# Kernel tuning notes

Measured on AMD Instinct MI355X. Metric: run time of the kernel, lower is better.

The kernel has to match this reference:

```python
import jax, jax.numpy as jnp
import numpy as np

N_NODES = 100000
N_EDGES = 3_200_000
F_IN, HID, N_CLS = 512, 16, 16


def setup_inputs() -> dict:
    key = jax.random.key(0)
    k1, k2, k3, k4 = jax.random.split(key, 4)
    x = jax.random.normal(k1, (N_NODES, F_IN), dtype=jnp.float32)
    edge_index = jax.random.randint(k2, (2, N_EDGES), 0, N_NODES, dtype=jnp.int64)
    W1 = jax.random.normal(k3, (F_IN, HID), dtype=jnp.float32) * 0.05
    b1 = jnp.zeros((HID,), dtype=jnp.float32)
    W2 = jax.random.normal(k4, (HID, N_CLS), dtype=jnp.float32) * 0.05
    b2 = jnp.zeros((N_CLS,), dtype=jnp.float32)
    return {"x": x, "edge_index": edge_index, "W1": W1, "b1": b1, "W2": W2, "b2": b2}


def _gcn_conv(x, W, b, row, col, norm, n_nodes):
    # GCNConv: linear first, then symmetric-normalized scatter-add aggregation
    h = x @ W                              # [N, out]
    msg = h[row] * norm[:, None]           # gather + scale, [E+N, out]
    out = jax.ops.segment_sum(msg, col, num_segments=n_nodes)
    return out + b


def reference(x, edge_index, W1, b1, W2, b2):
    n = x.shape[0]
    # add self-loops (GCNConv default)
    loop = jnp.arange(n, dtype=edge_index.dtype)
    row = jnp.concatenate([edge_index[0], loop])
    col = jnp.concatenate([edge_index[1], loop])
    # symmetric normalization D^-1/2 A D^-1/2 with edge_weight = 1
    deg = jax.ops.segment_sum(jnp.ones_like(col, dtype=x.dtype), col, num_segments=n)
    dinv = jnp.where(deg > 0, deg ** -0.5, 0.0)
    norm = dinv[row] * dinv[col]

    h = jax.nn.relu(_gcn_conv(x, W1, b1, row, col, norm, n))
    # dropout is identity in eval mode
    out = _gcn_conv(h, W2, b2, row, col, norm, n)
    return jax.nn.log_softmax(out, axis=-1)
```

## Files before the change

### kernel.cpp

```cpp
#include <hip/hip_runtime.h>
#include <hip/hip_fp16.h>

#define F_IN 512
#define BKT_BITS 7
#define NPB (1 << BKT_BITS)
#define NBMAX 1024
#define BWIN 5120
#define EPT 32
#define EPW (256 * EPT)

__global__ void k_init(int* __restrict__ cursor, int nb) {
    int i = blockIdx.x * blockDim.x + threadIdx.x;
    if (i < nb) cursor[i] = i * BWIN;
}

__global__ __launch_bounds__(256) void k_part(
    const int* __restrict__ row, const int* __restrict__ col,
    int* __restrict__ cursor, unsigned int* __restrict__ pairs, int E, int nb)
{
    __shared__ unsigned int staged[EPW];
    __shared__ unsigned short bkt[EPW];
    __shared__ int hist[NBMAX];
    __shared__ int sc[NBMAX];
    __shared__ int base[NBMAX];
    __shared__ int wsum[4];
    int tid = threadIdx.x;
    int lane = tid & 63;
    int e0 = blockIdx.x * EPW;
    for (int i = tid; i < nb; i += 256) hist[i] = 0;
    __syncthreads();

    int4 c4[EPT / 4];
    int rank[EPT];
    #pragma unroll
    for (int k = 0; k < EPT / 4; ++k) {
        int e = e0 + (tid + k * 256) * 4;
        if (e + 3 < E) {
            c4[k] = ((const int4*)col)[e >> 2];
        } else {
            c4[k].x = (e     < E) ? col[e]     : -1;
            c4[k].y = (e + 1 < E) ? col[e + 1] : -1;
            c4[k].z = (e + 2 < E) ? col[e + 2] : -1;
            c4[k].w = (e + 3 < E) ? col[e + 3] : -1;
        }
        const int* cc = (const int*)&c4[k];
        #pragma unroll
        for (int i = 0; i < 4; ++i)
            rank[4 * k + i] = (cc[i] >= 0) ? atomicAdd(&hist[cc[i] >> BKT_BITS], 1) : 0;
    }
    __syncthreads();

    int i0 = tid * 4;
    int a0 = 0, a1 = 0, a2 = 0, a3 = 0;
    {
        int h0 = (i0     < nb) ? hist[i0]     : 0;
        int h1 = (i0 + 1 < nb) ? hist[i0 + 1] : 0;
        int h2 = (i0 + 2 < nb) ? hist[i0 + 2] : 0;
        int h3 = (i0 + 3 < nb) ? hist[i0 + 3] : 0;
        base[i0]     = h0 ? atomicAdd(&cursor[i0],     h0) : 0;
        if (i0 + 1 < NBMAX) base[i0 + 1] = h1 ? atomicAdd(&cursor[i0 + 1], h1) : 0;
        if (i0 + 2 < NBMAX) base[i0 + 2] = h2 ? atomicAdd(&cursor[i0 + 2], h2) : 0;
        if (i0 + 3 < NBMAX) base[i0 + 3] = h3 ? atomicAdd(&cursor[i0 + 3], h3) : 0;
        a0 = h0; a1 = h1; a2 = h2; a3 = h3;
    }
    int s = a0 + a1 + a2 + a3;
    int ws = s;
    #pragma unroll
    for (int off = 1; off < 64; off <<= 1) {
        int t = __shfl_up(ws, off);
        if (lane >= off) ws += t;
    }
    if (lane == 63) wsum[tid >> 6] = ws;
    __syncthreads();
    int woff = 0;
    #pragma unroll
    for (int k = 0; k < 4; ++k) woff += (k < (tid >> 6)) ? wsum[k] : 0;
    int excl = woff + ws - s;
    sc[i0]     = excl + a0;
    sc[i0 + 1] = excl + a0 + a1;
    sc[i0 + 2] = excl + a0 + a1 + a2;
    sc[i0 + 3] = excl + s;
    __syncthreads();

    #pragma unroll
    for (int k = 0; k < EPT / 4; ++k) {
        int e = e0 + (tid + k * 256) * 4;
        int4 r4;
        if (e + 3 < E) {
            r4 = ((const int4*)row)[e >> 2];
        } else {
            r4.x = (e     < E) ? row[e]     : 0;
            r4.y = (e + 1 < E) ? row[e + 1] : 0;
            r4.z = (e + 2 < E) ? row[e + 2] : 0;
            r4.w = (e + 3 < E) ? row[e + 3] : 0;
        }
        const int* cc = (const int*)&c4[k];
        const int* rr = (const int*)&r4;
        #pragma unroll
        for (int i = 0; i < 4; ++i) {
            if (e + i >= E || cc[i] < 0) continue;
            int b = cc[i] >> BKT_BITS;
            int pos = (sc[b] - hist[b]) + rank[4 * k + i];
            staged[pos] = ((unsigned int)rr[i] << BKT_BITS)
                        | (unsigned int)(cc[i] & (NPB - 1));
            bkt[pos] = (unsigned short)b;
        }
    }
    __syncthreads();

    int vcnt = sc[nb - 1];
    for (int i = tid; i < vcnt; i += 256) {
        int b = bkt[i];
        int gpos = base[b] + (i - (sc[b] - hist[b]));
        if (gpos < (b + 1) * BWIN)
            pairs[gpos] = staged[i];
    }
}

__global__ __launch_bounds__(256) void k_csr(
    unsigned int* __restrict__ pairs, const int* __restrict__ cursor,
    int2* __restrict__ pd, float* __restrict__ dinv, int n, int nb)
{
    __shared__ int sorted[BWIN];
    __shared__ int hist[NPB];
    __shared__ int sc[NPB];
    __shared__ int curs[NPB];
    int b = blockIdx.x, tid = threadIdx.x;
    int n0 = b << BKT_BITS;
    int w0 = b * BWIN;
    int ec = min(cursor[b] - w0, BWIN);
    if (tid < NPB) hist[tid] = 0;
    __syncthreads();
    for (int e4 = tid; e4 < BWIN / 4; e4 += 256) {
        uint4 p4 = ((const uint4*)(pairs + w0))[e4];
        int e = e4 * 4;
        const unsigned int* pp = (const unsigned int*)&p4;
        #pragma unroll
        for (int i = 0; i < 4; ++i)
            if (e + i < ec) atomicAdd(&hist[pp[i] & (NPB - 1)], 1);
    }
    __syncthreads();
    if (tid < NPB) sc[tid] = hist[tid];
    __syncthreads();
    for (int off = 1; off < NPB; off <<= 1) {
        int t = (tid < NPB && tid >= off) ? sc[tid - off] : 0;
        __syncthreads();
        if (tid < NPB) sc[tid] += t;
        __syncthreads();
    }
    if (tid < NPB) {
        int st = sc[tid] - hist[tid];
        curs[tid] = st;
        int node = n0 + tid;
        if (node < n) {
            pd[node] = make_int2(w0 + st, hist[tid]);
            dinv[node] = rsqrtf((float)(hist[tid] + 1));
        }
    }
    __syncthreads();
    for (int e4 = tid; e4 < BWIN / 4; e4 += 256) {
        uint4 p4 = ((const uint4*)(pairs + w0))[e4];
        int e = e4 * 4;
        const unsigned int* pp = (const unsigned int*)&p4;
        #pragma unroll
        for (int i = 0; i < 4; ++i) {
            if (e + i < ec) {
                unsigned int p = pp[i];
                int pos = atomicAdd(&curs[p & (NPB - 1)], 1);
                sorted[pos] = (int)(p >> BKT_BITS);
            }
        }
    }
    __syncthreads();
    for (int i = tid; i < ec; i += 256)
        ((int*)pairs)[w0 + i] = sorted[i];
}

__global__ __launch_bounds__(256) void k_gemm1(
    const float* __restrict__ x, const float* __restrict__ W1,
    const float* __restrict__ dinv, __half2* __restrict__ hs, int n)
{
    __shared__ float red[4][64 * 17];
    const int lane = threadIdx.x & 63;
    const int wib  = threadIdx.x >> 6;
    const int wave = blockIdx.x * 4 + wib;
    const int nw   = gridDim.x * 4;
    float* rb = red[wib];

    float w[128];
    #pragma unroll
    for (int i = 0; i < 32; ++i) {
        float4 t = ((const float4*)W1)[lane * 32 + i];
        w[4*i+0] = t.x; w[4*i+1] = t.y; w[4*i+2] = t.z; w[4*i+3] = t.w;
    }
    const int q  = lane >> 4;
    const int jj = lane & 15;

    int node = wave;
    float4 a = {}, b = {};
    float di = 0.f;
    if (node < n) {
        const float4* xr = (const float4*)(x + (size_t)node * F_IN);
        a = xr[lane * 2];
        b = xr[lane * 2 + 1];
        di = dinv[node];
    }
    while (node < n) {
        int nxt = node + nw;
        float4 an = {}, bn = {};
        float dn = 0.f;
        if (nxt < n) {
            const float4* xr = (const float4*)(x + (size_t)nxt * F_IN);
            an = xr[lane * 2];
            bn = xr[lane * 2 + 1];
            dn = dinv[nxt];
        }
        float xs[8] = {a.x, a.y, a.z, a.w, b.x, b.y, b.z, b.w};
        float p[16];
        #pragma unroll
        for (int j = 0; j < 16; ++j) p[j] = 0.f;
        #pragma unroll
        for (int i = 0; i < 8; ++i)
            #pragma unroll
            for (int j = 0; j < 16; ++j)
                p[j] = fmaf(xs[i], w[i * 16 + j], p[j]);

        #pragma unroll
        for (int j = 0; j < 16; ++j) rb[lane * 17 + j] = p[j];
        __asm__ volatile("s_waitcnt lgkmcnt(0)" ::: "memory");
        float s = 0.f;
        #pragma unroll
        for (int i = 0; i < 16; ++i) s += rb[(q * 16 + i) * 17 + jj];
        s += __shfl_down(s, 32);
        s += __shfl_down(s, 16);

        float sv = s * di;
        float sn = __shfl_down(sv, 1);
        if (lane < 16 && (lane & 1) == 0) {
            __half2 hv = __halves2half2(__float2half(sv), __float2half(sn));
            hs[node * 8 + (lane >> 1)] = hv;
        }
        node = nxt; a = an; b = bn; di = dn;
    }
}

__global__ __launch_bounds__(256) void k_agg1(
    const __half2* __restrict__ hs, const int2* __restrict__ pd,
    const int* __restrict__ csr, const float* __restrict__ dinv,
    const float* __restrict__ b1, const float* __restrict__ W2,
    __half2* __restrict__ hs2, int n)
{
    int t = blockIdx.x * blockDim.x + threadIdx.x;
    int node = t >> 3, j2 = t & 7;
    if (node >= n) return;
    int2 p = pd[node];
    int e = p.x, s1 = p.x + p.y;
    float2 sum = __half22float2(hs[node * 8 + j2]);
    for (; e + 8 <= s1; e += 8) {
        int a0 = csr[e],   a1 = csr[e+1], a2 = csr[e+2], a3 = csr[e+3];
        int a4 = csr[e+4], a5 = csr[e+5], a6 = csr[e+6], a7 = csr[e+7];
        float2 v0 = __half22float2(hs[a0 * 8 + j2]);
        float2 v1 = __half22float2(hs[a1 * 8 + j2]);
        float2 v2 = __half22float2(hs[a2 * 8 + j2]);
        float2 v3 = __half22float2(hs[a3 * 8 + j2]);
        float2 v4 = __half22float2(hs[a4 * 8 + j2]);
        float2 v5 = __half22float2(hs[a5 * 8 + j2]);
        float2 v6 = __half22float2(hs[a6 * 8 + j2]);
        float2 v7 = __half22float2(hs[a7 * 8 + j2]);
        sum.x += ((v0.x+v1.x)+(v2.x+v3.x)) + ((v4.x+v5.x)+(v6.x+v7.x));
        sum.y += ((v0.y+v1.y)+(v2.y+v3.y)) + ((v4.y+v5.y)+(v6.y+v7.y));
    }
    for (; e < s1; ++e) {
        float2 v = __half22float2(hs[csr[e] * 8 + j2]);
        sum.x += v.x; sum.y += v.y;
    }
    float di = dinv[node];
    float2 b1v = ((const float2*)b1)[j2];
    float va = fmaxf(fmaf(sum.x, di, b1v.x), 0.f);
    float vb = fmaxf(fmaf(sum.y, di, b1v.y), 0.f);
    float ha = 0.f, hb = 0.f;
    #pragma unroll
    for (int k2 = 0; k2 < 8; ++k2) {
        float oa = __shfl(va, k2, 8);
        float ob = __shfl(vb, k2, 8);
        ha = fmaf(oa, W2[(2*k2)   * 16 + 2*j2],     ha);
        hb = fmaf(oa, W2[(2*k2)   * 16 + 2*j2 + 1], hb);
        ha = fmaf(ob, W2[(2*k2+1) * 16 + 2*j2],     ha);
        hb = fmaf(ob, W2[(2*k2+1) * 16 + 2*j2 + 1], hb);
    }
    hs2[node * 8 + j2] = __halves2half2(__float2half(ha * di), __float2half(hb * di));
}

__global__ __launch_bounds__(256) void k_agg2(
    const __half2* __restrict__ hs2, const int2* __restrict__ pd,
    const int* __restrict__ csr, const float* __restrict__ dinv,
    const float* __restrict__ b2, float2* __restrict__ out, int n)
{
    int t = blockIdx.x * blockDim.x + threadIdx.x;
    int node = t >> 3, j2 = t & 7;
    if (node >= n) return;
    int2 p = pd[node];
    int e = p.x, s1 = p.x + p.y;
    float2 sum = __half22float2(hs2[node * 8 + j2]);
    for (; e + 8 <= s1; e += 8) {
        int a0 = csr[e],   a1 = csr[e+1], a2 = csr[e+2], a3 = csr[e+3];
        int a4 = csr[e+4], a5 = csr[e+5], a6 = csr[e+6], a7 = csr[e+7];
        float2 v0 = __half22float2(hs2[a0 * 8 + j2]);
        float2 v1 = __half22float2(hs2[a1 * 8 + j2]);
        float2 v2 = __half22float2(hs2[a2 * 8 + j2]);
        float2 v3 = __half22float2(hs2[a3 * 8 + j2]);
        float2 v4 = __half22float2(hs2[a4 * 8 + j2]);
        float2 v5 = __half22float2(hs2[a5 * 8 + j2]);
        float2 v6 = __half22float2(hs2[a6 * 8 + j2]);
        float2 v7 = __half22float2(hs2[a7 * 8 + j2]);
        sum.x += ((v0.x+v1.x)+(v2.x+v3.x)) + ((v4.x+v5.x)+(v6.x+v7.x));
        sum.y += ((v0.y+v1.y)+(v2.y+v3.y)) + ((v4.y+v5.y)+(v6.y+v7.y));
    }
    for (; e < s1; ++e) {
        float2 v = __half22float2(hs2[csr[e] * 8 + j2]);
        sum.x += v.x; sum.y += v.y;
    }
    float di = dinv[node];
    float2 b2v = ((const float2*)b2)[j2];
    float vx = fmaf(sum.x, di, b2v.x);
    float vy = fmaf(sum.y, di, b2v.y);
    float m = fmaxf(vx, vy);
    #pragma unroll
    for (int off = 4; off >= 1; off >>= 1) m = fmaxf(m, __shfl_xor(m, off));
    float s = expf(vx - m) + expf(vy - m);
    #pragma unroll
    for (int off = 4; off >= 1; off >>= 1) s += __shfl_xor(s, off);
    float ls = logf(s);
    out[node * 8 + j2] = make_float2(vx - m - ls, vy - m - ls);
}

extern "C" void kernel_launch(void* const* d_in, const int* in_sizes, int n_in,
                              void* d_out, int out_size, void* d_ws, size_t ws_size,
                              hipStream_t stream)
{
    const float* x  = (const float*)d_in[0];
    const int*   ei = (const int*)d_in[1];
    const float* W1 = (const float*)d_in[2];
    const float* b1 = (const float*)d_in[3];
    const float* W2 = (const float*)d_in[4];
    const float* b2 = (const float*)d_in[5];
    float* out = (float*)d_out;

    const int n = in_sizes[0] / F_IN;
    const int E = in_sizes[1] / 2;
    const int nb = (n + NPB - 1) >> BKT_BITS;

    char* ws = (char*)d_ws;
    size_t o = 0;
    #define ALIGN512(s) (((s) + 511) & ~(size_t)511)
    float* dinv = (float*)(ws + o);           o += ALIGN512((size_t)n * 4);
    int2*  pd   = (int2*)(ws + o);            o += ALIGN512((size_t)n * 8);
    int*   curs = (int*)(ws + o);             o += ALIGN512((size_t)NBMAX * 4);
    unsigned int* pairs = (unsigned int*)(ws + o);
    o += ALIGN512((size_t)nb * BWIN * 4);
    __half2* hs  = (__half2*)(ws + o);        o += ALIGN512((size_t)n * 16 * 2);
    __half2* hs2 = (__half2*)(ws + o);        o += ALIGN512((size_t)n * 16 * 2);
    #undef ALIGN512

    k_init<<<(nb + 255) / 256, 256, 0, stream>>>(curs, nb);
    k_part<<<(E + EPW - 1) / EPW, 256, 0, stream>>>(ei, ei + E, curs, pairs, E, nb);
    k_csr <<<nb, 256, 0, stream>>>(pairs, curs, pd, dinv, n, nb);

    k_gemm1<<<2048, 256, 0, stream>>>(x, W1, dinv, hs, n);
    k_agg1 <<<(n * 8 + 255) / 256, 256, 0, stream>>>(hs, pd, (const int*)pairs,
                                                     dinv, b1, W2, hs2, n);
    k_agg2 <<<(n * 8 + 255) / 256, 256, 0, stream>>>(hs2, pd, (const int*)pairs,
                                                     dinv, b2, (float2*)out, n);
}
```

Baseline: 434.7 us.

## Fuse all stages into one persistent kernel with software grid barriers

Replaces the six separate launches (init, partition, CSR build, GEMM, two aggregations) with one persistent kernel. It sizes the grid from occupancy and separates phases with an atomic-counter grid barrier, and shared memory is unioned across phases. Cursor init becomes a memset, with cursors now relative to each bucket. The aim is to remove launch gaps and tail effects between stages. In exchange, the partition and GEMM phases run on fewer blocks, register pressure rises under launch_bounds(256,2), and the software barrier adds its own cost and a deadlock risk if not all blocks are co-resident.

```diff
diff --git a/kernel.cpp b/kernel.cpp
--- a/kernel.cpp
+++ b/kernel.cpp
@@ -9,329 +9,352 @@
 #define EPT 32
 #define EPW (256 * EPT)
 
-__global__ void k_init(int* __restrict__ cursor, int nb) {
-    int i = blockIdx.x * blockDim.x + threadIdx.x;
-    if (i < nb) cursor[i] = i * BWIN;
+union SU {
+    struct {
+        unsigned int staged[EPW];
+        unsigned short bkt[EPW];
+        int hist[NBMAX];
+        int sc[NBMAX];
+        int base[NBMAX];
+        int wsum[4];
+    } p;
+    struct {
+        int sorted[BWIN];
+        int hist[NPB];
+        int sc[NPB];
+        int curs[NPB];
+    } c;
+    struct {
+        float red[4][64 * 17];
+    } g;
+};
+
+__device__ __forceinline__ void gbar(int* cnt, int* gen, int nblk) {
+    __syncthreads();
+    if (threadIdx.x == 0) {
+        __threadfence();
+        int g = __hip_atomic_load(gen, __ATOMIC_RELAXED, __HIP_MEMORY_SCOPE_AGENT);
+        if (__hip_atomic_fetch_add(cnt, 1, __ATOMIC_RELAXED,
+                                   __HIP_MEMORY_SCOPE_AGENT) == nblk - 1) {
+            __hip_atomic_store(cnt, 0, __ATOMIC_RELAXED, __HIP_MEMORY_SCOPE_AGENT);
+            __hip_atomic_store(gen, g + 1, __ATOMIC_RELEASE, __HIP_MEMORY_SCOPE_AGENT);
+        } else {
+            while (__hip_atomic_load(gen, __ATOMIC_RELAXED,
+                                     __HIP_MEMORY_SCOPE_AGENT) == g)
+                __builtin_amdgcn_s_sleep(8);
+        }
+        __threadfence();
+    }
+    __syncthreads();
 }
 
-__global__ __launch_bounds__(256) void k_part(
-    const int* __restrict__ row, const int* __restrict__ col,
-    int* __restrict__ cursor, unsigned int* __restrict__ pairs, int E, int nb)
+__global__ __launch_bounds__(256, 2) void k_fused(
+    const float* __restrict__ x, const int* __restrict__ ei,
+    const float* __restrict__ W1, const float* __restrict__ b1,
+    const float* __restrict__ W2, const float* __restrict__ b2,
+    float2* __restrict__ out,
+    float* __restrict__ dinv, int2* __restrict__ pd, int* __restrict__ cursor,
+    int* __restrict__ bar, unsigned int* __restrict__ pairs,
+    __half2* __restrict__ hs, __half2* __restrict__ hs2,
+    int n, int E, int nb, int nslice)
 {
-    __shared__ unsigned int staged[EPW];
-    __shared__ unsigned short bkt[EPW];
-    __shared__ int hist[NBMAX];
-    __shared__ int sc[NBMAX];
-    __shared__ int base[NBMAX];
-    __shared__ int wsum[4];
-    int tid = threadIdx.x;
-    int lane = tid & 63;
-    int e0 = blockIdx.x * EPW;
-    for (int i = tid; i < nb; i += 256) hist[i] = 0;
-    __syncthreads();
-
-    int4 c4[EPT / 4];
-    int rank[EPT];
-    #pragma unroll
-    for (int k = 0; k < EPT / 4; ++k) {
-        int e = e0 + (tid + k * 256) * 4;
-        if (e + 3 < E) {
-            c4[k] = ((const int4*)col)[e >> 2];
-        } else {
-            c4[k].x = (e     < E) ? col[e]     : -1;
-            c4[k].y = (e + 1 < E) ? col[e + 1] : -1;
-            c4[k].z = (e + 2 < E) ? col[e + 2] : -1;
-            c4[k].w = (e + 3 < E) ? col[e + 3] : -1;
-        }
-        const int* cc = (const int*)&c4[k];
+    __shared__ SU sh;
+    const int tid  = threadIdx.x;
+    const int lane = tid & 63;
+    const int gsz  = gridDim.x * 256;
+    const int* row = ei;
+    const int* col = ei + E;
+
+    for (int s = blockIdx.x; s < nslice; s += gridDim.x) {
+        int e0 = s * EPW;
+        for (int i = tid; i < nb; i += 256) sh.p.hist[i] = 0;
+        __syncthreads();
+
+        int4 c4[EPT / 4];
+        int rank[EPT];
         #pragma unroll
-        for (int i = 0; i < 4; ++i)
-            rank[4 * k + i] = (cc[i] >= 0) ? atomicAdd(&hist[cc[i] >> BKT_BITS], 1) : 0;
-    }
-    __syncthreads();
-
-    int i0 = tid * 4;
-    int a0 = 0, a1 = 0, a2 = 0, a3 = 0;
+        for (int k = 0; k < EPT / 4; ++k) {
+            int e = e0 + (tid + k * 256) * 4;
+            if (e + 3 < E) {
+                c4[k] = ((const int4*)col)[e >> 2];
+            } else {
+                c4[k].x = (e     < E) ? col[e]     : -1;
+                c4[k].y = (e + 1 < E) ? col[e + 1] : -1;
+                c4[k].z = (e + 2 < E) ? col[e + 2] : -1;
+                c4[k].w = (e + 3 < E) ? col[e + 3] : -1;
+            }
+            const int* cc = (const int*)&c4[k];
+            #pragma unroll
+            for (int i = 0; i < 4; ++i)
+                rank[4 * k + i] = (cc[i] >= 0)
+                    ? atomicAdd(&sh.p.hist[cc[i] >> BKT_BITS], 1) : 0;
+        }
+        __syncthreads();
+
+        int i0 = tid * 4;
+        int h0 = (i0     < nb) ? sh.p.hist[i0]     : 0;
+        int h1 = (i0 + 1 < nb) ? sh.p.hist[i0 + 1] : 0;
+        int h2 = (i0 + 2 < nb) ? sh.p.hist[i0 + 2] : 0;
+        int h3 = (i0 + 3 < nb) ? sh.p.hist[i0 + 3] : 0;
+        sh.p.base[i0]     = h0 ? i0 * BWIN       + atomicAdd(&cursor[i0],     h0) : 0;
+        sh.p.base[i0 + 1] = h1 ? (i0 + 1) * BWIN + atomicAdd(&cursor[i0 + 1], h1) : 0;
+        sh.p.base[i0 + 2] = h2 ? (i0 + 2) * BWIN + atomicAdd(&cursor[i0 + 2], h2) : 0;
+        sh.p.base[i0 + 3] = h3 ? (i0 + 3) * BWIN + atomicAdd(&cursor[i0 + 3], h3) : 0;
+        int ssum = h0 + h1 + h2 + h3;
+        int ws = ssum;
+        #pragma unroll
+        for (int off = 1; off < 64; off <<= 1) {
+            int t = __shfl_up(ws, off);
+            if (lane >= off) ws += t;
+        }
+        if (lane == 63) sh.p.wsum[tid >> 6] = ws;
+        __syncthreads();
+        int woff = 0;
+        #pragma unroll
+        for (int k = 0; k < 4; ++k) woff += (k < (tid >> 6)) ? sh.p.wsum[k] : 0;
+        int excl = woff + ws - ssum;
+        sh.p.sc[i0]     = excl + h0;
+        sh.p.sc[i0 + 1] = excl + h0 + h1;
+        sh.p.sc[i0 + 2] = excl + h0 + h1 + h2;
+        sh.p.sc[i0 + 3] = excl + ssum;
+        __syncthreads();
+
+        #pragma unroll
+        for (int k = 0; k < EPT / 4; ++k) {
+            int e = e0 + (tid + k * 256) * 4;
+            int4 r4;
+            if (e + 3 < E) {
+                r4 = ((const int4*)row)[e >> 2];
+            } else {
+                r4.x = (e     < E) ? row[e]     : 0;
+                r4.y = (e + 1 < E) ? row[e + 1] : 0;
+                r4.z = (e + 2 < E) ? row[e + 2] : 0;
+                r4.w = (e + 3 < E) ? row[e + 3] : 0;
+            }
+            const int* cc = (const int*)&c4[k];
+            const int* rr = (const int*)&r4;
+            #pragma unroll
+            for (int i = 0; i < 4; ++i) {
+                if (e + i >= E || cc[i] < 0) continue;
+                int b = cc[i] >> BKT_BITS;
+                int pos = (sh.p.sc[b] - sh.p.hist[b]) + rank[4 * k + i];
+                sh.p.staged[pos] = ((unsigned int)rr[i] << BKT_BITS)
+                                 | (unsigned int)(cc[i] & (NPB - 1));
+                sh.p.bkt[pos] = (unsigned short)b;
+            }
+        }
+        __syncthreads();
+
+        int vcnt = sh.p.sc[nb - 1];
+        for (int i = tid; i < vcnt; i += 256) {
+            int b = sh.p.bkt[i];
+            int gpos = sh.p.base[b] + (i - (sh.p.sc[b] - sh.p.hist[b]));
+            if (gpos < (b + 1) * BWIN)
+                pairs[gpos] = sh.p.staged[i];
+        }
+        __syncthreads();
+    }
+    gbar(bar, bar + 1, gridDim.x);
+
+    for (int b = blockIdx.x; b < nb; b += gridDim.x) {
+        int n0 = b << BKT_BITS;
+        int w0 = b * BWIN;
+        int ec = min(cursor[b], BWIN);
+        if (tid < NPB) sh.c.hist[tid] = 0;
+        __syncthreads();
+        for (int e4 = tid; e4 < BWIN / 4; e4 += 256) {
+            uint4 p4 = ((const uint4*)(pairs + w0))[e4];
+            int e = e4 * 4;
+            const unsigned int* pp = (const unsigned int*)&p4;
+            #pragma unroll
+            for (int i = 0; i < 4; ++i)
+                if (e + i < ec) atomicAdd(&sh.c.hist[pp[i] & (NPB - 1)], 1);
+        }
+        __syncthreads();
+        if (tid < NPB) sh.c.sc[tid] = sh.c.hist[tid];
+        __syncthreads();
+        for (int off = 1; off < NPB; off <<= 1) {
+            int t = (tid < NPB && tid >= off) ? sh.c.sc[tid - off] : 0;
+            __syncthreads();
+            if (tid < NPB) sh.c.sc[tid] += t;
+            __syncthreads();
+        }
+        if (tid < NPB) {
+            int st = sh.c.sc[tid] - sh.c.hist[tid];
+            sh.c.curs[tid] = st;
+            int node = n0 + tid;
+            if (node < n) {
+                pd[node] = make_int2(w0 + st, sh.c.hist[tid]);
+                dinv[node] = rsqrtf((float)(sh.c.hist[tid] + 1));
+            }
+        }
+        __syncthreads();
+        for (int e4 = tid; e4 < BWIN / 4; e4 += 256) {
+            uint4 p4 = ((const uint4*)(pairs + w0))[e4];
+            int e = e4 * 4;
+            const unsigned int* pp = (const unsigned int*)&p4;
+            #pragma unroll
+            for (int i = 0; i < 4; ++i) {
+                if (e + i < ec) {
+                    unsigned int p = pp[i];
+                    int pos = atomicAdd(&sh.c.curs[p & (NPB - 1)], 1);
+                    sh.c.sorted[pos] = (int)(p >> BKT_BITS);
+                }
+            }
+        }
+        __syncthreads();
+        for (int i = tid; i < ec; i += 256)
+            ((int*)pairs)[w0 + i] = sh.c.sorted[i];
+        __syncthreads();
+    }
+    gbar(bar, bar + 1, gridDim.x);
+
     {
-        int h0 = (i0     < nb) ? hist[i0]     : 0;
-        int h1 = (i0 + 1 < nb) ? hist[i0 + 1] : 0;
-        int h2 = (i0 + 2 < nb) ? hist[i0 + 2] : 0;
-        int h3 = (i0 + 3 < nb) ? hist[i0 + 3] : 0;
-        base[i0]     = h0 ? atomicAdd(&cursor[i0],     h0) : 0;
-        if (i0 + 1 < NBMAX) base[i0 + 1] = h1 ? atomicAdd(&cursor[i0 + 1], h1) : 0;
-        if (i0 + 2 < NBMAX) base[i0 + 2] = h2 ? atomicAdd(&cursor[i0 + 2], h2) : 0;
-        if (i0 + 3 < NBMAX) base[i0 + 3] = h3 ? atomicAdd(&cursor[i0 + 3], h3) : 0;
-        a0 = h0; a1 = h1; a2 = h2; a3 = h3;
-    }
-    int s = a0 + a1 + a2 + a3;
-    int ws = s;
-    #pragma unroll
-    for (int off = 1; off < 64; off <<= 1) {
-        int t = __shfl_up(ws, off);
-        if (lane >= off) ws += t;
-    }
-    if (lane == 63) wsum[tid >> 6] = ws;
-    __syncthreads();
-    int woff = 0;
-    #pragma unroll
-    for (int k = 0; k < 4; ++k) woff += (k < (tid >> 6)) ? wsum[k] : 0;
-    int excl = woff + ws - s;
-    sc[i0]     = excl + a0;
-    sc[i0 + 1] = excl + a0 + a1;
-    sc[i0 + 2] = excl + a0 + a1 + a2;
-    sc[i0 + 3] = excl + s;
-    __syncthreads();
-
-    #pragma unroll
-    for (int k = 0; k < EPT / 4; ++k) {
-        int e = e0 + (tid + k * 256) * 4;
-        int4 r4;
-        if (e + 3 < E) {
-            r4 = ((const int4*)row)[e >> 2];
-        } else {
-            r4.x = (e     < E) ? row[e]     : 0;
-            r4.y = (e + 1 < E) ? row[e + 1] : 0;
-            r4.z = (e + 2 < E) ? row[e + 2] : 0;
-            r4.w = (e + 3 < E) ? row[e + 3] : 0;
-        }
-        const int* cc = (const int*)&c4[k];
-        const int* rr = (const int*)&r4;
+        const int wib = tid >> 6;
+        float* rb = sh.g.red[wib];
+        float w[128];
         #pragma unroll
-        for (int i = 0; i < 4; ++i) {
-            if (e + i >= E || cc[i] < 0) continue;
-            int b = cc[i] >> BKT_BITS;
-            int pos = (sc[b] - hist[b]) + rank[4 * k + i];
-            staged[pos] = ((unsigned int)rr[i] << BKT_BITS)
-                        | (unsigned int)(cc[i] & (NPB - 1));
-            bkt[pos] = (unsigned short)b;
-        }
-    }
-    __syncthreads();
-
-    int vcnt = sc[nb - 1];
-    for (int i = tid; i < vcnt; i += 256) {
-        int b = bkt[i];
-        int gpos = base[b] + (i - (sc[b] - hist[b]));
-        if (gpos < (b + 1) * BWIN)
-            pairs[gpos] = staged[i];
-    }
-}
-
-__global__ __launch_bounds__(256) void k_csr(
-    unsigned int* __restrict__ pairs, const int* __restrict__ cursor,
-    int2* __restrict__ pd, float* __restrict__ dinv, int n, int nb)
-{
-    __shared__ int sorted[BWIN];
-    __shared__ int hist[NPB];
-    __shared__ int sc[NPB];
-    __shared__ int curs[NPB];
-    int b = blockIdx.x, tid = threadIdx.x;
-    int n0 = b << BKT_BITS;
-    int w0 = b * BWIN;
-    int ec = min(cursor[b] - w0, BWIN);
-    if (tid < NPB) hist[tid] = 0;
-    __syncthreads();
-    for (int e4 = tid; e4 < BWIN / 4; e4 += 256) {
-        uint4 p4 = ((const uint4*)(pairs + w0))[e4];
-        int e = e4 * 4;
-        const unsigned int* pp = (const unsigned int*)&p4;
-        #pragma unroll
-        for (int i = 0; i < 4; ++i)
-            if (e + i < ec) atomicAdd(&hist[pp[i] & (NPB - 1)], 1);
-    }
-    __syncthreads();
-    if (tid < NPB) sc[tid] = hist[tid];
-    __syncthreads();
-    for (int off = 1; off < NPB; off <<= 1) {
-        int t = (tid < NPB && tid >= off) ? sc[tid - off] : 0;
-        __syncthreads();
-        if (tid < NPB) sc[tid] += t;
-        __syncthreads();
-    }
-    if (tid < NPB) {
-        int st = sc[tid] - hist[tid];
-        curs[tid] = st;
-        int node = n0 + tid;
+        for (int i = 0; i < 32; ++i) {
+            float4 t = ((const float4*)W1)[lane * 32 + i];
+            w[4*i+0] = t.x; w[4*i+1] = t.y; w[4*i+2] = t.z; w[4*i+3] = t.w;
+        }
+        const int q  = lane >> 4;
+        const int jj = lane & 15;
+        const int nw = gridDim.x * 4;
+
+        int node = blockIdx.x * 4 + wib;
+        float4 a = {}, b = {};
+        float di = 0.f;
         if (node < n) {
-            pd[node] = make_int2(w0 + st, hist[tid]);
-            dinv[node] = rsqrtf((float)(hist[tid] + 1));
-        }
-    }
-    __syncthreads();
-    for (int e4 = tid; e4 < BWIN / 4; e4 += 256) {
-        uint4 p4 = ((const uint4*)(pairs + w0))[e4];
-        int e = e4 * 4;
-        const unsigned int* pp = (const unsigned int*)&p4;
-        #pragma unroll
-        for (int i = 0; i < 4; ++i) {
-            if (e + i < ec) {
-                unsigned int p = pp[i];
-                int pos = atomicAdd(&curs[p & (NPB - 1)], 1);
-                sorted[pos] = (int)(p >> BKT_BITS);
-            }
-        }
-    }
-    __syncthreads();
-    for (int i = tid; i < ec; i += 256)
-        ((int*)pairs)[w0 + i] = sorted[i];
-}
-
-__global__ __launch_bounds__(256) void k_gemm1(
-    const float* __restrict__ x, const float* __restrict__ W1,
-    const float* __restrict__ dinv, __half2* __restrict__ hs, int n)
-{
-    __shared__ float red[4][64 * 17];
-    const int lane = threadIdx.x & 63;
-    const int wib  = threadIdx.x >> 6;
-    const int wave = blockIdx.x * 4 + wib;
-    const int nw   = gridDim.x * 4;
-    float* rb = red[wib];
-
-    float w[128];
-    #pragma unroll
-    for (int i = 0; i < 32; ++i) {
-        float4 t = ((const float4*)W1)[lane * 32 + i];
-        w[4*i+0] = t.x; w[4*i+1] = t.y; w[4*i+2] = t.z; w[4*i+3] = t.w;
-    }
-    const int q  = lane >> 4;
-    const int jj = lane & 15;
-
-    int node = wave;
-    float4 a = {}, b = {};
-    float di = 0.f;
-    if (node < n) {
-        const float4* xr = (const float4*)(x + (size_t)node * F_IN);
-        a = xr[lane * 2];
-        b = xr[lane * 2 + 1];
-        di = dinv[node];
-    }
-    while (node < n) {
-        int nxt = node + nw;
-        float4 an = {}, bn = {};
-        float dn = 0.f;
-        if (nxt < n) {
-            const float4* xr = (const float4*)(x + (size_t)nxt * F_IN);
-            an = xr[lane * 2];
-            bn = xr[lane * 2 + 1];
-            dn = dinv[nxt];
-        }
-        float xs[8] = {a.x, a.y, a.z, a.w, b.x, b.y, b.z, b.w};
-        float p[16];
-        #pragma unroll
-        for (int j = 0; j < 16; ++j) p[j] = 0.f;
-        #pragma unroll
-        for (int i = 0; i < 8; ++i)
-            #pragma unroll
-            for (int j = 0; j < 16; ++j)
-                p[j] = fmaf(xs[i], w[i * 16 + j], p[j]);
-
-        #pragma unroll
-        for (int j = 0; j < 16; ++j) rb[lane * 17 + j] = p[j];
-        __asm__ volatile("s_waitcnt lgkmcnt(0)" ::: "memory");
-        float s = 0.f;
-        #pragma unroll
-        for (int i = 0; i < 16; ++i) s += rb[(q * 16 + i) * 17 + jj];
-        s += __shfl_down(s, 32);
-        s += __shfl_down(s, 16);
-
-        float sv = s * di;
-        float sn = __shfl_down(sv, 1);
-        if (lane < 16 && (lane & 1) == 0) {
-            __half2 hv = __halves2half2(__float2half(sv), __float2half(sn));
-            hs[node * 8 + (lane >> 1)] = hv;
-        }
-        node = nxt; a = an; b = bn; di = dn;
-    }
-}
-
-__global__ __launch_bounds__(256) void k_agg1(
-    const __half2* __restrict__ hs, const int2* __restrict__ pd,
-    const int* __restrict__ csr, const float* __restrict__ dinv,
-    const float* __restrict__ b1, const float* __restrict__ W2,
-    __half2* __restrict__ hs2, int n)
-{
-    int t = blockIdx.x * blockDim.x + threadIdx.x;
-    int node = t >> 3, j2 = t & 7;
-    if (node >= n) return;
-    int2 p = pd[node];
-    int e = p.x, s1 = p.x + p.y;
-    float2 sum = __half22float2(hs[node * 8 + j2]);
-    for (; e + 8 <= s1; e += 8) {
-        int a0 = csr[e],   a1 = csr[e+1], a2 = csr[e+2], a3 = csr[e+3];
-        int a4 = csr[e+4], a5 = csr[e+5], a6 = csr[e+6], a7 = csr[e+7];
-        float2 v0 = __half22float2(hs[a0 * 8 + j2]);
-        float2 v1 = __half22float2(hs[a1 * 8 + j2]);
-        float2 v2 = __half22float2(hs[a2 * 8 + j2]);
-        float2 v3 = __half22float2(hs[a3 * 8 + j2]);
-        float2 v4 = __half22float2(hs[a4 * 8 + j2]);
-        float2 v5 = __half22float2(hs[a5 * 8 + j2]);
-        float2 v6 = __half22float2(hs[a6 * 8 + j2]);
-        float2 v7 = __half22float2(hs[a7 * 8 + j2]);
-        sum.x += ((v0.x+v1.x)+(v2.x+v3.x)) + ((v4.x+v5.x)+(v6.x+v7.x));
-        sum.y += ((v0.y+v1.y)+(v2.y+v3.y)) + ((v4.y+v5.y)+(v6.y+v7.y));
-    }
-    for (; e < s1; ++e) {
-        float2 v = __half22float2(hs[csr[e] * 8 + j2]);
-        sum.x += v.x; sum.y += v.y;
-    }
-    float di = dinv[node];
-    float2 b1v = ((const float2*)b1)[j2];
-    float va = fmaxf(fmaf(sum.x, di, b1v.x), 0.f);
-    float vb = fmaxf(fmaf(sum.y, di, b1v.y), 0.f);
-    float ha = 0.f, hb = 0.f;
-    #pragma unroll
-    for (int k2 = 0; k2 < 8; ++k2) {
-        float oa = __shfl(va, k2, 8);
-        float ob = __shfl(vb, k2, 8);
-        ha = fmaf(oa, W2[(2*k2)   * 16 + 2*j2],     ha);
-        hb = fmaf(oa, W2[(2*k2)   * 16 + 2*j2 + 1], hb);
-        ha = fmaf(ob, W2[(2*k2+1) * 16 + 2*j2],     ha);
-        hb = fmaf(ob, W2[(2*k2+1) * 16 + 2*j2 + 1], hb);
-    }
-    hs2[node * 8 + j2] = __halves2half2(__float2half(ha * di), __float2half(hb * di));
-}
-
-__global__ __launch_bounds__(256) void k_agg2(
-    const __half2* __restrict__ hs2, const int2* __restrict__ pd,
-    const int* __restrict__ csr, const float* __restrict__ dinv,
-    const float* __restrict__ b2, float2* __restrict__ out, int n)
-{
-    int t = blockIdx.x * blockDim.x + threadIdx.x;
-    int node = t >> 3, j2 = t & 7;
-    if (node >= n) return;
-    int2 p = pd[node];
-    int e = p.x, s1 = p.x + p.y;
-    float2 sum = __half22float2(hs2[node * 8 + j2]);
-    for (; e + 8 <= s1; e += 8) {
-        int a0 = csr[e],   a1 = csr[e+1], a2 = csr[e+2], a3 = csr[e+3];
-        int a4 = csr[e+4], a5 = csr[e+5], a6 = csr[e+6], a7 = csr[e+7];
-        float2 v0 = __half22float2(hs2[a0 * 8 + j2]);
-        float2 v1 = __half22float2(hs2[a1 * 8 + j2]);
-        float2 v2 = __half22float2(hs2[a2 * 8 + j2]);
-        float2 v3 = __half22float2(hs2[a3 * 8 + j2]);
-        float2 v4 = __half22float2(hs2[a4 * 8 + j2]);
-        float2 v5 = __half22float2(hs2[a5 * 8 + j2]);
-        float2 v6 = __half22float2(hs2[a6 * 8 + j2]);
-        float2 v7 = __half22float2(hs2[a7 * 8 + j2]);
-        sum.x += ((v0.x+v1.x)+(v2.x+v3.x)) + ((v4.x+v5.x)+(v6.x+v7.x));
-        sum.y += ((v0.y+v1.y)+(v2.y+v3.y)) + ((v4.y+v5.y)+(v6.y+v7.y));
-    }
-    for (; e < s1; ++e) {
-        float2 v = __half22float2(hs2[csr[e] * 8 + j2]);
-        sum.x += v.x; sum.y += v.y;
-    }
-    float di = dinv[node];
-    float2 b2v = ((const float2*)b2)[j2];
-    float vx = fmaf(sum.x, di, b2v.x);
-    float vy = fmaf(sum.y, di, b2v.y);
-    float m = fmaxf(vx, vy);
-    #pragma unroll
-    for (int off = 4; off >= 1; off >>= 1) m = fmaxf(m, __shfl_xor(m, off));
-    float s = expf(vx - m) + expf(vy - m);
-    #pragma unroll
-    for (int off = 4; off >= 1; off >>= 1) s += __shfl_xor(s, off);
-    float ls = logf(s);
-    out[node * 8 + j2] = make_float2(vx - m - ls, vy - m - ls);
+            const float4* xr = (const float4*)(x + (size_t)node * F_IN);
+            a = xr[lane * 2];
+            b = xr[lane * 2 + 1];
+            di = dinv[node];
+        }
+        while (node < n) {
+            int nxt = node + nw;
+            float4 an = {}, bn = {};
+            float dn = 0.f;
+            if (nxt < n) {
+                const float4* xr = (const float4*)(x + (size_t)nxt * F_IN);
+                an = xr[lane * 2];
+                bn = xr[lane * 2 + 1];
+                dn = dinv[nxt];
+            }
+            float xs[8] = {a.x, a.y, a.z, a.w, b.x, b.y, b.z, b.w};
+            float p[16];
+            #pragma unroll
+            for (int j = 0; j < 16; ++j) p[j] = 0.f;
+            #pragma unroll
+            for (int i = 0; i < 8; ++i)
+                #pragma unroll
+                for (int j = 0; j < 16; ++j)
+                    p[j] = fmaf(xs[i], w[i * 16 + j], p[j]);
+
+            #pragma unroll
+            for (int j = 0; j < 16; ++j) rb[lane * 17 + j] = p[j];
+            __asm__ volatile("s_waitcnt lgkmcnt(0)" ::: "memory");
+            float s = 0.f;
+            #pragma unroll
+            for (int i = 0; i < 16; ++i) s += rb[(q * 16 + i) * 17 + jj];
+            s += __shfl_down(s, 32);
+            s += __shfl_down(s, 16);
+
+            float sv = s * di;
+            float sn = __shfl_down(sv, 1);
+            if (lane < 16 && (lane & 1) == 0) {
+                __half2 hv = __halves2half2(__float2half(sv), __float2half(sn));
+                hs[node * 8 + (lane >> 1)] = hv;
+            }
+            node = nxt; a = an; b = bn; di = dn;
+        }
+    }
+    gbar(bar, bar + 1, gridDim.x);
+
+    {
+        const int* csr = (const int*)pairs;
+        for (int it = blockIdx.x * 256 + tid; it < n * 8; it += gsz) {
+            int node = it >> 3, j2 = it & 7;
+            int2 p = pd[node];
+            int e = p.x, s1 = p.x + p.y;
+            float2 sum = __half22float2(hs[node * 8 + j2]);
+            for (; e + 8 <= s1; e += 8) {
+                int a0 = csr[e],   a1 = csr[e+1], a2 = csr[e+2], a3 = csr[e+3];
+                int a4 = csr[e+4], a5 = csr[e+5], a6 = csr[e+6], a7 = csr[e+7];
+                float2 v0 = __half22float2(hs[a0 * 8 + j2]);
+                float2 v1 = __half22float2(hs[a1 * 8 + j2]);
+                float2 v2 = __half22float2(hs[a2 * 8 + j2]);
+                float2 v3 = __half22float2(hs[a3 * 8 + j2]);
+                float2 v4 = __half22float2(hs[a4 * 8 + j2]);
+                float2 v5 = __half22float2(hs[a5 * 8 + j2]);
+                float2 v6 = __half22float2(hs[a6 * 8 + j2]);
+                float2 v7 = __half22float2(hs[a7 * 8 + j2]);
+                sum.x += ((v0.x+v1.x)+(v2.x+v3.x)) + ((v4.x+v5.x)+(v6.x+v7.x));
+                sum.y += ((v0.y+v1.y)+(v2.y+v3.y)) + ((v4.y+v5.y)+(v6.y+v7.y));
+            }
+            for (; e < s1; ++e) {
+                float2 v = __half22float2(hs[csr[e] * 8 + j2]);
+                sum.x += v.x; sum.y += v.y;
+            }
+            float di = dinv[node];
+            float2 b1v = ((const float2*)b1)[j2];
+            float va = fmaxf(fmaf(sum.x, di, b1v.x), 0.f);
+            float vb = fmaxf(fmaf(sum.y, di, b1v.y), 0.f);
+            float ha = 0.f, hb = 0.f;
+            #pragma unroll
+            for (int k2 = 0; k2 < 8; ++k2) {
+                float oa = __shfl(va, k2, 8);
+                float ob = __shfl(vb, k2, 8);
+                ha = fmaf(oa, W2[(2*k2)   * 16 + 2*j2],     ha);
+                hb = fmaf(oa, W2[(2*k2)   * 16 + 2*j2 + 1], hb);
+                ha = fmaf(ob, W2[(2*k2+1) * 16 + 2*j2],     ha);
+                hb = fmaf(ob, W2[(2*k2+1) * 16 + 2*j2 + 1], hb);
+            }
+            hs2[node * 8 + j2] =
+                __halves2half2(__float2half(ha * di), __float2half(hb * di));
+        }
+    }
+    gbar(bar, bar + 1, gridDim.x);
+
+    {
+        const int* csr = (const int*)pairs;
+        for (int it = blockIdx.x * 256 + tid; it < n * 8; it += gsz) {
+            int node = it >> 3, j2 = it & 7;
+            int2 p = pd[node];
+            int e = p.x, s1 = p.x + p.y;
+            float2 sum = __half22float2(hs2[node * 8 + j2]);
+            for (; e + 8 <= s1; e += 8) {
+                int a0 = csr[e],   a1 = csr[e+1], a2 = csr[e+2], a3 = csr[e+3];
+                int a4 = csr[e+4], a5 = csr[e+5], a6 = csr[e+6], a7 = csr[e+7];
+                float2 v0 = __half22float2(hs2[a0 * 8 + j2]);
+                float2 v1 = __half22float2(hs2[a1 * 8 + j2]);
+                float2 v2 = __half22float2(hs2[a2 * 8 + j2]);
+                float2 v3 = __half22float2(hs2[a3 * 8 + j2]);
+                float2 v4 = __half22float2(hs2[a4 * 8 + j2]);
+                float2 v5 = __half22float2(hs2[a5 * 8 + j2]);
+                float2 v6 = __half22float2(hs2[a6 * 8 + j2]);
+                float2 v7 = __half22float2(hs2[a7 * 8 + j2]);
+                sum.x += ((v0.x+v1.x)+(v2.x+v3.x)) + ((v4.x+v5.x)+(v6.x+v7.x));
+                sum.y += ((v0.y+v1.y)+(v2.y+v3.y)) + ((v4.y+v5.y)+(v6.y+v7.y));
+            }
+            for (; e < s1; ++e) {
+                float2 v = __half22float2(hs2[csr[e] * 8 + j2]);
+                sum.x += v.x; sum.y += v.y;
+            }
+            float di = dinv[node];
+            float2 b2v = ((const float2*)b2)[j2];
+            float vx = fmaf(sum.x, di, b2v.x);
+            float vy = fmaf(sum.y, di, b2v.y);
+            float m = fmaxf(vx, vy);
+            #pragma unroll
+            for (int off = 4; off >= 1; off >>= 1) m = fmaxf(m, __shfl_xor(m, off));
+            float s = expf(vx - m) + expf(vy - m);
+            #pragma unroll
+            for (int off = 4; off >= 1; off >>= 1) s += __shfl_xor(s, off);
+            float ls = logf(s);
+            out[node * 8 + j2] = make_float2(vx - m - ls, vy - m - ls);
+        }
+    }
 }
 
 extern "C" void kernel_launch(void* const* d_in, const int* in_sizes, int n_in,
@@ -349,6 +372,7 @@
     const int n = in_sizes[0] / F_IN;
     const int E = in_sizes[1] / 2;
     const int nb = (n + NPB - 1) >> BKT_BITS;
+    const int nslice = (E + EPW - 1) / EPW;
 
     char* ws = (char*)d_ws;
     size_t o = 0;
@@ -356,19 +380,27 @@
     float* dinv = (float*)(ws + o);           o += ALIGN512((size_t)n * 4);
     int2*  pd   = (int2*)(ws + o);            o += ALIGN512((size_t)n * 8);
     int*   curs = (int*)(ws + o);             o += ALIGN512((size_t)NBMAX * 4);
+    int*   bar  = (int*)(ws + o);             o += 512;
     unsigned int* pairs = (unsigned int*)(ws + o);
     o += ALIGN512((size_t)nb * BWIN * 4);
     __half2* hs  = (__half2*)(ws + o);        o += ALIGN512((size_t)n * 16 * 2);
     __half2* hs2 = (__half2*)(ws + o);        o += ALIGN512((size_t)n * 16 * 2);
     #undef ALIGN512
 
-    k_init<<<(nb + 255) / 256, 256, 0, stream>>>(curs, nb);
-    k_part<<<(E + EPW - 1) / EPW, 256, 0, stream>>>(ei, ei + E, curs, pairs, E, nb);
-    k_csr <<<nb, 256, 0, stream>>>(pairs, curs, pd, dinv, n, nb);
-
-    k_gemm1<<<2048, 256, 0, stream>>>(x, W1, dinv, hs, n);
-    k_agg1 <<<(n * 8 + 255) / 256, 256, 0, stream>>>(hs, pd, (const int*)pairs,
-                                                     dinv, b1, W2, hs2, n);
-    k_agg2 <<<(n * 8 + 255) / 256, 256, 0, stream>>>(hs2, pd, (const int*)pairs,
-                                                     dinv, b2, (float2*)out, n);
+    static int g_grid = 0;
+    if (g_grid == 0) {
+        int occ = 0;
+        hipOccupancyMaxActiveBlocksPerMultiprocessor(&occ, k_fused, 256, 0);
+        int ncu = 0;
+        hipDeviceGetAttribute(&ncu, hipDeviceAttributeMultiprocessorCount, 0);
+        if (occ < 1) occ = 1;
+        if (ncu < 1) ncu = 256;
+        g_grid = occ * ncu;
+        if (g_grid > 2048) g_grid = 2048;
+    }
+
+    hipMemsetAsync(curs, 0, (size_t)NBMAX * 4 + 512, stream);
+    k_fused<<<g_grid, 256, 0, stream>>>(x, ei, W1, b1, W2, b2, (float2*)out,
+                                        dinv, pd, curs, bar, pairs, hs, hs2,
+                                        n, E, nb, nslice);
 }
```

Result: slower. 649.9 us (+49.5%).

## Pack W1 registers as half2 in gemm1, bound CSR loops by edge count

Applied to the files above, without the earlier changes.

In k_gemm1 the per-lane copy of W1 is now held as 64 half2 registers instead of 128 floats, and launch bounds ask for 4 blocks per SM, which cuts register pressure and raises occupancy for the memory-bound x read. Each half2 is converted back to float before the FMA, so this adds conversion instructions and rounds the weights to fp16. In k_csr the two loops over the bucket window now stop at the real edge count instead of scanning the full BWIN, which skips wasted loads. The k_part edit only renames variables.

```diff
diff --git a/kernel.cpp b/kernel.cpp
--- a/kernel.cpp
+++ b/kernel.cpp
@@ -51,20 +51,16 @@
     __syncthreads();
 
     int i0 = tid * 4;
-    int a0 = 0, a1 = 0, a2 = 0, a3 = 0;
-    {
-        int h0 = (i0     < nb) ? hist[i0]     : 0;
-        int h1 = (i0 + 1 < nb) ? hist[i0 + 1] : 0;
-        int h2 = (i0 + 2 < nb) ? hist[i0 + 2] : 0;
-        int h3 = (i0 + 3 < nb) ? hist[i0 + 3] : 0;
-        base[i0]     = h0 ? atomicAdd(&cursor[i0],     h0) : 0;
-        if (i0 + 1 < NBMAX) base[i0 + 1] = h1 ? atomicAdd(&cursor[i0 + 1], h1) : 0;
-        if (i0 + 2 < NBMAX) base[i0 + 2] = h2 ? atomicAdd(&cursor[i0 + 2], h2) : 0;
-        if (i0 + 3 < NBMAX) base[i0 + 3] = h3 ? atomicAdd(&cursor[i0 + 3], h3) : 0;
-        a0 = h0; a1 = h1; a2 = h2; a3 = h3;
-    }
-    int s = a0 + a1 + a2 + a3;
-    int ws = s;
+    int h0 = (i0     < nb) ? hist[i0]     : 0;
+    int h1 = (i0 + 1 < nb) ? hist[i0 + 1] : 0;
+    int h2 = (i0 + 2 < nb) ? hist[i0 + 2] : 0;
+    int h3 = (i0 + 3 < nb) ? hist[i0 + 3] : 0;
+    base[i0]     = h0 ? atomicAdd(&cursor[i0],     h0) : 0;
+    if (i0 + 1 < NBMAX) base[i0 + 1] = h1 ? atomicAdd(&cursor[i0 + 1], h1) : 0;
+    if (i0 + 2 < NBMAX) base[i0 + 2] = h2 ? atomicAdd(&cursor[i0 + 2], h2) : 0;
+    if (i0 + 3 < NBMAX) base[i0 + 3] = h3 ? atomicAdd(&cursor[i0 + 3], h3) : 0;
+    int ssum = h0 + h1 + h2 + h3;
+    int ws = ssum;
     #pragma unroll
     for (int off = 1; off < 64; off <<= 1) {
         int t = __shfl_up(ws, off);
@@ -75,11 +71,11 @@
     int woff = 0;
     #pragma unroll
     for (int k = 0; k < 4; ++k) woff += (k < (tid >> 6)) ? wsum[k] : 0;
-    int excl = woff + ws - s;
-    sc[i0]     = excl + a0;
-    sc[i0 + 1] = excl + a0 + a1;
-    sc[i0 + 2] = excl + a0 + a1 + a2;
-    sc[i0 + 3] = excl + s;
+    int excl = woff + ws - ssum;
+    sc[i0]     = excl + h0;
+    sc[i0 + 1] = excl + h0 + h1;
+    sc[i0 + 2] = excl + h0 + h1 + h2;
+    sc[i0 + 3] = excl + ssum;
     __syncthreads();
 
     #pragma unroll
@@ -129,9 +125,10 @@
     int n0 = b << BKT_BITS;
     int w0 = b * BWIN;
     int ec = min(cursor[b] - w0, BWIN);
+    int ec4 = (ec + 3) >> 2;
     if (tid < NPB) hist[tid] = 0;
     __syncthreads();
-    for (int e4 = tid; e4 < BWIN / 4; e4 += 256) {
+    for (int e4 = tid; e4 < ec4; e4 += 256) {
         uint4 p4 = ((const uint4*)(pairs + w0))[e4];
         int e = e4 * 4;
         const unsigned int* pp = (const unsigned int*)&p4;
@@ -158,7 +155,7 @@
         }
     }
     __syncthreads();
-    for (int e4 = tid; e4 < BWIN / 4; e4 += 256) {
+    for (int e4 = tid; e4 < ec4; e4 += 256) {
         uint4 p4 = ((const uint4*)(pairs + w0))[e4];
         int e = e4 * 4;
         const unsigned int* pp = (const unsigned int*)&p4;
@@ -176,7 +173,7 @@
         ((int*)pairs)[w0 + i] = sorted[i];
 }
 
-__global__ __launch_bounds__(256) void k_gemm1(
+__global__ __launch_bounds__(256, 4) void k_gemm1(
     const float* __restrict__ x, const float* __restrict__ W1,
     const float* __restrict__ dinv, __half2* __restrict__ hs, int n)
 {
@@ -187,11 +184,12 @@
     const int nw   = gridDim.x * 4;
     float* rb = red[wib];
 
-    float w[128];
+    __half2 w2[64];
     #pragma unroll
     for (int i = 0; i < 32; ++i) {
         float4 t = ((const float4*)W1)[lane * 32 + i];
-        w[4*i+0] = t.x; w[4*i+1] = t.y; w[4*i+2] = t.z; w[4*i+3] = t.w;
+        w2[2*i]   = __floats2half2_rn(t.x, t.y);
+        w2[2*i+1] = __floats2half2_rn(t.z, t.w);
     }
     const int q  = lane >> 4;
     const int jj = lane & 15;
@@ -220,10 +218,14 @@
         #pragma unroll
         for (int j = 0; j < 16; ++j) p[j] = 0.f;
         #pragma unroll
-        for (int i = 0; i < 8; ++i)
+        for (int i = 0; i < 8; ++i) {
             #pragma unroll
-            for (int j = 0; j < 16; ++j)
-                p[j] = fmaf(xs[i], w[i * 16 + j], p[j]);
+            for (int jp = 0; jp < 8; ++jp) {
+                float2 wv = __half22float2(w2[i * 8 + jp]);
+                p[2*jp]   = fmaf(xs[i], wv.x, p[2*jp]);
+                p[2*jp+1] = fmaf(xs[i], wv.y, p[2*jp+1]);
+            }
+        }
 
         #pragma unroll
         for (int j = 0; j < 16; ++j) rb[lane * 17 + j] = p[j];
```

Result: slower. 577.8 us (+32.9%).
